# Optimization experiments

Measured on AMD Instinct MI355X. Metric: run time of the kernel, lower is better.

The kernel has to match this reference:

```python
import jax, jax.numpy as jnp
import numpy as np

D_MODEL = 1024
N_HEADS = 16
HEAD_DIM = D_MODEL // N_HEADS


def setup_inputs() -> dict:
    key = jax.random.key(0)
    ks = jax.random.split(key, 5)
    scale = 1.0 / np.sqrt(D_MODEL)
    x = jax.random.normal(ks[0], (2, 2048, D_MODEL), dtype=jnp.float32)
    Wq = jax.random.normal(ks[1], (D_MODEL, D_MODEL), dtype=jnp.float32) * scale
    Wk = jax.random.normal(ks[2], (D_MODEL, D_MODEL), dtype=jnp.float32) * scale
    Wv = jax.random.normal(ks[3], (D_MODEL, D_MODEL), dtype=jnp.float32) * scale
    Wo = jax.random.normal(ks[4], (D_MODEL, D_MODEL), dtype=jnp.float32) * scale
    return {"x": x, "Wq": Wq, "Wk": Wk, "Wv": Wv, "Wo": Wo}


def reference(x, Wq, Wk, Wv, Wo):
    # x: [B, S, D]; weights stored as [out, in] like nn.Linear -> y = x @ W.T
    B, S, D = x.shape
    H, Hd = N_HEADS, HEAD_DIM
    attn_scale = 1.0 / np.sqrt(Hd)

    def split_heads(t):  # [B,S,D] -> [B,H,S,Hd]
        return t.reshape(B, S, H, Hd).transpose(0, 2, 1, 3)

    q = split_heads(x @ Wq.T)
    k = split_heads(x @ Wk.T)
    v = split_heads(x @ Wv.T)

    scores = jnp.einsum('bhqd,bhkd->bhqk', q, k) * attn_scale  # [B,H,S,S]
    causal = jnp.tril(jnp.ones((S, S), dtype=bool))
    scores = jnp.where(causal, scores, jnp.finfo(scores.dtype).min)
    attn = jax.nn.softmax(scores, axis=-1)
    out = jnp.einsum('bhqk,bhkd->bhqd', attn, v)  # [B,H,S,Hd]
    out = out.transpose(0, 2, 1, 3).reshape(B, S, D)
    return out @ Wo.T
```

## Files before the change

kernel.cpp:

```cpp
#include <hip/hip_runtime.h>
#include <hip/hip_bf16.h>

typedef __attribute__((ext_vector_type(8))) __bf16 bf16x8;
typedef __attribute__((ext_vector_type(4))) __bf16 bf16x4;
typedef __attribute__((ext_vector_type(4))) float f32x4;

#define D_MODEL 1024
#define S_LEN   2048
#define BATCH   2
#define NH      16
#define HD      64
#define MROWS   (BATCH * S_LEN)

#define EXP2F(x) __builtin_amdgcn_exp2f(x)

__global__ __launch_bounds__(256) void cvt_bf16(const float* __restrict__ in,
                                                __bf16* __restrict__ out, int n4) {
    int i = blockIdx.x * 256 + threadIdx.x;
    if (i < n4) {
        float4 v = ((const float4*)in)[i];
        bf16x4 o = {(__bf16)v.x, (__bf16)v.y, (__bf16)v.z, (__bf16)v.w};
        ((bf16x4*)out)[i] = o;
    }
}

__global__ __launch_bounds__(256) void cvt_w3(const float* __restrict__ Wq,
                                              const float* __restrict__ Wk,
                                              const float* __restrict__ Wv,
                                              __bf16* __restrict__ out) {
    const int per = (D_MODEL * D_MODEL) / 4;
    int i = blockIdx.x * 256 + threadIdx.x;
    int sel = i / per;
    int off = i - sel * per;
    const float* src = (sel == 0) ? Wq : (sel == 1) ? Wk : Wv;
    float4 v = ((const float4*)src)[off];
    bf16x4 o = {(__bf16)v.x, (__bf16)v.y, (__bf16)v.z, (__bf16)v.w};
    ((bf16x4*)out)[i] = o;
}

__device__ __forceinline__ void g2l16(const void* g, __bf16* l) {
    __builtin_amdgcn_global_load_lds((const __attribute__((address_space(1))) void*)g,
                                     (__attribute__((address_space(3))) void*)l, 16, 0, 0);
}

__global__ __launch_bounds__(256) void gemm_qkv(const __bf16* __restrict__ A,
                                                const __bf16* __restrict__ W,
                                                __bf16* __restrict__ Qb,
                                                __bf16* __restrict__ Kq,
                                                __bf16* __restrict__ VTb,
                                                float qs) {
    __shared__ __bf16 sa[128 * 64];
    __shared__ __bf16 sb[128 * 64];

    const int t    = threadIdx.x;
    const int lane = t & 63;
    const int wid  = t >> 6;
    const int lr   = lane & 15;
    const int lg   = lane >> 4;
    const int wr   = wid >> 1;
    const int wc   = wid & 1;
    const int K    = D_MODEL;
    const int m0   = blockIdx.y * 128;
    const int n0   = blockIdx.x * 128;

    const __bf16* Ab = A + (size_t)m0 * K;
    const __bf16* Wb = W + (size_t)n0 * K;

    f32x4 acc[4][4];
#pragma unroll
    for (int m = 0; m < 4; m++)
#pragma unroll
        for (int n = 0; n < 4; n++) acc[m][n] = (f32x4){0.f, 0.f, 0.f, 0.f};

    for (int k0 = 0; k0 < K; k0 += 64) {
#pragma unroll
        for (int i = 0; i < 4; i++) {
            int ca = i * 256 + t;
            int row = ca >> 3;
            int sc  = ((ca & 7) ^ (row & 7)) * 8;
            g2l16(&Ab[(size_t)row * K + k0 + sc], &sa[ca * 8]);
            g2l16(&Wb[(size_t)row * K + k0 + sc], &sb[ca * 8]);
        }
        __syncthreads();

        bf16x8 af[4][2], bfr[4][2];
#pragma unroll
        for (int m = 0; m < 4; m++) {
            const int row = wr * 64 + m * 16 + lr;
#pragma unroll
            for (int kc = 0; kc < 2; kc++)
                af[m][kc] = *(const bf16x8*)&sa[row * 64 + (((kc * 4 + lg) ^ (lr & 7)) * 8)];
        }
#pragma unroll
        for (int n = 0; n < 4; n++) {
            const int row = wc * 64 + n * 16 + lr;
#pragma unroll
            for (int kc = 0; kc < 2; kc++)
                bfr[n][kc] = *(const bf16x8*)&sb[row * 64 + (((kc * 4 + lg) ^ (lr & 7)) * 8)];
        }
#pragma unroll
        for (int m = 0; m < 4; m++)
#pragma unroll
            for (int n = 0; n < 4; n++)
#pragma unroll
                for (int kc = 0; kc < 2; kc++)
                    acc[m][n] = __builtin_amdgcn_mfma_f32_16x16x32_bf16(af[m][kc], bfr[n][kc], acc[m][n], 0, 0, 0);
        __syncthreads();
    }

#pragma unroll
    for (int m = 0; m < 4; m++) {
#pragma unroll
        for (int n = 0; n < 4; n++) {
#pragma unroll
            for (int j = 0; j < 4; j++) {
                int row = m0 + wr * 64 + m * 16 + lg * 4 + j;
                int col = n0 + wc * 64 + n * 16 + lr;
                float v = acc[m][n][j];
                if (col < 1024) {
                    Qb[(size_t)row * D_MODEL + col] = (__bf16)(v * qs);
                } else if (col < 2048) {
                    Kq[(size_t)row * D_MODEL + col - 1024] = (__bf16)v;
                } else {
                    int c2 = col - 2048;
                    int b = row >> 11, s = row & 2047;
                    int h = c2 >> 6, d = c2 & 63;
                    VTb[(((size_t)(b * NH + h) * HD + d) << 11) + s] = (__bf16)v;
                }
            }
        }
    }
}

__global__ __launch_bounds__(256) void gemm_out(const __bf16* __restrict__ A,
                                                const __bf16* __restrict__ W,
                                                float* __restrict__ C,
                                                int M, int N, int K) {
    __shared__ __bf16 sa[128 * 64];
    __shared__ __bf16 sb[64 * 64];

    const int t    = threadIdx.x;
    const int lane = t & 63;
    const int wid  = t >> 6;
    const int lr   = lane & 15;
    const int lg   = lane >> 4;
    const int wr   = wid >> 1;
    const int wc   = wid & 1;
    const int m0   = blockIdx.y * 128;
    const int n0   = blockIdx.x * 64;

    const __bf16* Ab = A + (size_t)m0 * K;
    const __bf16* Wb = W + (size_t)n0 * K;

    f32x4 acc[4][2];
#pragma unroll
    for (int m = 0; m < 4; m++)
#pragma unroll
        for (int n = 0; n < 2; n++) acc[m][n] = (f32x4){0.f, 0.f, 0.f, 0.f};

    for (int k0 = 0; k0 < K; k0 += 64) {
#pragma unroll
        for (int i = 0; i < 4; i++) {
            int ca = i * 256 + t;
            int row = ca >> 3;
            int sc  = ((ca & 7) ^ (row & 7)) * 8;
            g2l16(&Ab[(size_t)row * K + k0 + sc], &sa[ca * 8]);
        }
#pragma unroll
        for (int i = 0; i < 2; i++) {
            int ca = i * 256 + t;
            int row = ca >> 3;
            int sc  = ((ca & 7) ^ (row & 7)) * 8;
            g2l16(&Wb[(size_t)row * K + k0 + sc], &sb[ca * 8]);
        }
        __syncthreads();

        bf16x8 af[4][2], bfr[2][2];
#pragma unroll
        for (int m = 0; m < 4; m++) {
            const int row = wr * 64 + m * 16 + lr;
#pragma unroll
            for (int kc = 0; kc < 2; kc++)
                af[m][kc] = *(const bf16x8*)&sa[row * 64 + (((kc * 4 + lg) ^ (lr & 7)) * 8)];
        }
#pragma unroll
        for (int n = 0; n < 2; n++) {
            const int row = wc * 32 + n * 16 + lr;
#pragma unroll
            for (int kc = 0; kc < 2; kc++)
                bfr[n][kc] = *(const bf16x8*)&sb[row * 64 + (((kc * 4 + lg) ^ (lr & 7)) * 8)];
        }
#pragma unroll
        for (int m = 0; m < 4; m++)
#pragma unroll
            for (int n = 0; n < 2; n++)
#pragma unroll
                for (int kc = 0; kc < 2; kc++)
                    acc[m][n] = __builtin_amdgcn_mfma_f32_16x16x32_bf16(af[m][kc], bfr[n][kc], acc[m][n], 0, 0, 0);
        __syncthreads();
    }

#pragma unroll
    for (int m = 0; m < 4; m++)
#pragma unroll
        for (int n = 0; n < 2; n++)
#pragma unroll
            for (int j = 0; j < 4; j++) {
                int row = m0 + wr * 64 + m * 16 + lg * 4 + j;
                int col = n0 + wc * 32 + n * 16 + lr;
                C[(size_t)row * N + col] = acc[m][n][j];
            }
}

__global__ __launch_bounds__(256) void attn_fwd(const __bf16* __restrict__ Q,
                                                const __bf16* __restrict__ Kb,
                                                const __bf16* __restrict__ VT,
                                                __bf16* __restrict__ O) {
    __shared__ __bf16 kt[2][64 * 64];
    __shared__ __bf16 vt[2][64 * 64];
    __shared__ __bf16 pt[4][16][72];

    const int t    = threadIdx.x;
    const int lane = t & 63;
    const int wid  = t >> 6;
    const int lr   = lane & 15;
    const int lg   = lane >> 4;
    const int bid  = blockIdx.x;
    const int qb   = 31 - (bid >> 5);
    const int bh   = bid & 31;
    const int b    = bh >> 4;
    const int h    = bh & 15;
    const int col  = h * HD;

    const size_t qrow = (size_t)b * S_LEN + qb * 64 + wid * 16;
    const int q_lo = qb * 64 + wid * 16 + lg * 4;
    const __bf16* Kbase = Kb + (size_t)b * S_LEN * D_MODEL + col;
    const __bf16* Vbase = VT + (size_t)bh * HD * S_LEN;

    const int ca0 = t, ca1 = t + 256;
    const int r0 = ca0 >> 3, s0 = ((ca0 & 7) ^ (r0 & 7)) * 8;
    const int r1 = ca1 >> 3, s1 = ((ca1 & 7) ^ (r1 & 7)) * 8;

    bf16x8 qf[2];
#pragma unroll
    for (int c = 0; c < 2; c++)
        qf[c] = *(const bf16x8*)&Q[(qrow + lr) * D_MODEL + col + c * 32 + lg * 8];

    f32x4 o[4];
#pragma unroll
    for (int n = 0; n < 4; n++) o[n] = (f32x4){0.f, 0.f, 0.f, 0.f};
    float psum[4] = {0.f, 0.f, 0.f, 0.f};

    g2l16(&Kbase[(size_t)r0 * D_MODEL + s0], &kt[0][ca0 * 8]);
    g2l16(&Kbase[(size_t)r1 * D_MODEL + s1], &kt[0][ca1 * 8]);
    g2l16(&Vbase[(size_t)r0 * S_LEN + s0],   &vt[0][ca0 * 8]);
    g2l16(&Vbase[(size_t)r1 * S_LEN + s1],   &vt[0][ca1 * 8]);
    __syncthreads();

    for (int kvt = 0; kvt <= qb; kvt++) {
        const int kv0 = kvt * 64;
        const int cur = kvt & 1;
        const bool diag = (kvt == qb);

        if (kvt < qb) {
            const int nb = cur ^ 1;
            const int kv1 = kv0 + 64;
            g2l16(&Kbase[(size_t)(kv1 + r0) * D_MODEL + s0], &kt[nb][ca0 * 8]);
            g2l16(&Kbase[(size_t)(kv1 + r1) * D_MODEL + s1], &kt[nb][ca1 * 8]);
            g2l16(&Vbase[(size_t)r0 * S_LEN + kv1 + s0],     &vt[nb][ca0 * 8]);
            g2l16(&Vbase[(size_t)r1 * S_LEN + kv1 + s1],     &vt[nb][ca1 * 8]);
        }

        f32x4 s[4];
        __builtin_amdgcn_s_setprio(1);
#pragma unroll
        for (int tt = 0; tt < 4; tt++) {
            s[tt] = (f32x4){0.f, 0.f, 0.f, 0.f};
#pragma unroll
            for (int c = 0; c < 2; c++) {
                const int row = tt * 16 + lr;
                bf16x8 kf = *(const bf16x8*)&kt[cur][row * 64 + (((c * 4 + lg) ^ (lr & 7)) * 8)];
                s[tt] = __builtin_amdgcn_mfma_f32_16x16x32_bf16(qf[c], kf, s[tt], 0, 0, 0);
            }
        }
        __builtin_amdgcn_s_setprio(0);

        if (diag) {
#pragma unroll
            for (int tt = 0; tt < 4; tt++) {
                int kg = kv0 + tt * 16 + lr;
#pragma unroll
                for (int j = 0; j < 4; j++)
                    if (kg > q_lo + j) s[tt][j] = -1e30f;
            }
        }

#pragma unroll
        for (int tt = 0; tt < 4; tt++) {
#pragma unroll
            for (int j = 0; j < 4; j++) {
                float p = EXP2F(s[tt][j]);
                psum[j] += p;
                pt[wid][lg * 4 + j][tt * 16 + lr] = (__bf16)p;
            }
        }

        asm volatile("s_waitcnt lgkmcnt(0)" ::: "memory");
        __builtin_amdgcn_sched_barrier(0);

        __builtin_amdgcn_s_setprio(1);
#pragma unroll
        for (int c = 0; c < 2; c++) {
            bf16x8 pa = *(const bf16x8*)&pt[wid][lr][c * 32 + lg * 8];
#pragma unroll
            for (int n = 0; n < 4; n++) {
                const int d = n * 16 + lr;
                bf16x8 vf = *(const bf16x8*)&vt[cur][d * 64 + (((c * 4 + lg) ^ (lr & 7)) * 8)];
                o[n] = __builtin_amdgcn_mfma_f32_16x16x32_bf16(pa, vf, o[n], 0, 0, 0);
            }
        }
        __builtin_amdgcn_s_setprio(0);

        __syncthreads();
    }

#pragma unroll
    for (int j = 0; j < 4; j++) {
#pragma unroll
        for (int off = 1; off < 16; off <<= 1)
            psum[j] += __shfl_xor(psum[j], off, 64);
        psum[j] = 1.0f / psum[j];
    }

#pragma unroll
    for (int n = 0; n < 4; n++) {
#pragma unroll
        for (int j = 0; j < 4; j++) {
            float val = o[n][j] * psum[j];
            O[(qrow + lg * 4 + j) * D_MODEL + col + n * 16 + lr] = (__bf16)val;
        }
    }
}

extern "C" void kernel_launch(void* const* d_in, const int* in_sizes, int n_in,
                              void* d_out, int out_size, void* d_ws, size_t ws_size,
                              hipStream_t stream) {
    const float* x  = (const float*)d_in[0];
    const float* Wq = (const float*)d_in[1];
    const float* Wk = (const float*)d_in[2];
    const float* Wv = (const float*)d_in[3];
    const float* Wo = (const float*)d_in[4];
    float* out = (float*)d_out;

    const size_t XE = (size_t)MROWS * D_MODEL;
    const size_t WE = (size_t)D_MODEL * D_MODEL;
    __bf16* xb  = (__bf16*)d_ws;
    __bf16* Qb  = xb + XE;
    __bf16* Kq  = Qb + XE;
    __bf16* VTb = Kq + XE;
    __bf16* AO  = xb;

    __bf16* wqkv = (__bf16*)d_out;
    __bf16* wob  = Qb;

    cvt_bf16<<<(int)(XE / 4 / 256), 256, 0, stream>>>(x, xb, (int)(XE / 4));
    cvt_w3<<<(int)(3 * WE / 4 / 256), 256, 0, stream>>>(Wq, Wk, Wv, wqkv);

    const float qs = 0.125f * 1.44269504088896340736f;
    gemm_qkv<<<dim3(3 * D_MODEL / 128, MROWS / 128), 256, 0, stream>>>(xb, wqkv, Qb, Kq, VTb, qs);

    attn_fwd<<<1024, 256, 0, stream>>>(Qb, Kq, VTb, AO);

    cvt_bf16<<<(int)(WE / 4 / 256), 256, 0, stream>>>(Wo, wob, (int)(WE / 4));
    gemm_out<<<dim3(D_MODEL / 64, MROWS / 128), 256, 0, stream>>>(AO, wob, out, MROWS, D_MODEL, D_MODEL);
}
```

Measured before the change: 118.3 us.

## Process 128 query rows per attention block and fuse input conversions

Each attention wave now handles two 16-row query chunks, so one block covers 128 query rows. Every K/V tile loaded into LDS is therefore reused across twice as many queries, and the grid shrinks from 1024 to 512 blocks. The x and Wq/Wk/Wv fp32-to-bf16 conversions are merged into a single launch to save one kernel launch. The trade-offs are higher register pressure, fewer blocks to balance the uneven causal work, and some waves spending MFMA work on fully masked diagonal tiles.

```diff
diff --git a/kernel.cpp b/kernel.cpp
--- a/kernel.cpp
+++ b/kernel.cpp
@@ -24,18 +24,30 @@
     }
 }
 
-__global__ __launch_bounds__(256) void cvt_w3(const float* __restrict__ Wq,
-                                              const float* __restrict__ Wk,
-                                              const float* __restrict__ Wv,
-                                              __bf16* __restrict__ out) {
-    const int per = (D_MODEL * D_MODEL) / 4;
+__global__ __launch_bounds__(256) void cvt_all(const float* __restrict__ x,
+                                               const float* __restrict__ Wq,
+                                               const float* __restrict__ Wk,
+                                               const float* __restrict__ Wv,
+                                               __bf16* __restrict__ xb,
+                                               __bf16* __restrict__ wqkv) {
+    const int nx = (MROWS * D_MODEL) / 4;
+    const int nw = (D_MODEL * D_MODEL) / 4;
     int i = blockIdx.x * 256 + threadIdx.x;
-    int sel = i / per;
-    int off = i - sel * per;
-    const float* src = (sel == 0) ? Wq : (sel == 1) ? Wk : Wv;
-    float4 v = ((const float4*)src)[off];
+    const float* src;
+    __bf16* dst;
+    int si, di;
+    if (i < nx) {
+        src = x; si = i; dst = xb; di = i;
+    } else {
+        int k = i - nx;
+        int sel = k / nw;
+        si = k - sel * nw;
+        src = (sel == 0) ? Wq : (sel == 1) ? Wk : Wv;
+        dst = wqkv; di = k;
+    }
+    float4 v = ((const float4*)src)[si];
     bf16x4 o = {(__bf16)v.x, (__bf16)v.y, (__bf16)v.z, (__bf16)v.w};
-    ((bf16x4*)out)[i] = o;
+    ((bf16x4*)dst)[di] = o;
 }
 
 __device__ __forceinline__ void g2l16(const void* g, __bf16* l) {
@@ -226,14 +238,13 @@
     const int lr   = lane & 15;
     const int lg   = lane >> 4;
     const int bid  = blockIdx.x;
-    const int qb   = 31 - (bid >> 5);
+    const int qb   = 15 - (bid >> 5);
     const int bh   = bid & 31;
     const int b    = bh >> 4;
     const int h    = bh & 15;
     const int col  = h * HD;
 
-    const size_t qrow = (size_t)b * S_LEN + qb * 64 + wid * 16;
-    const int q_lo = qb * 64 + wid * 16 + lg * 4;
+    const size_t qrowb = (size_t)b * S_LEN + qb * 128 + wid * 32;
     const __bf16* Kbase = Kb + (size_t)b * S_LEN * D_MODEL + col;
     const __bf16* Vbase = VT + (size_t)bh * HD * S_LEN;
 
@@ -241,15 +252,19 @@
     const int r0 = ca0 >> 3, s0 = ((ca0 & 7) ^ (r0 & 7)) * 8;
     const int r1 = ca1 >> 3, s1 = ((ca1 & 7) ^ (r1 & 7)) * 8;
 
-    bf16x8 qf[2];
-#pragma unroll
-    for (int c = 0; c < 2; c++)
-        qf[c] = *(const bf16x8*)&Q[(qrow + lr) * D_MODEL + col + c * 32 + lg * 8];
-
-    f32x4 o[4];
-#pragma unroll
-    for (int n = 0; n < 4; n++) o[n] = (f32x4){0.f, 0.f, 0.f, 0.f};
-    float psum[4] = {0.f, 0.f, 0.f, 0.f};
+    bf16x8 qf[2][2];
+#pragma unroll
+    for (int hc = 0; hc < 2; hc++)
+#pragma unroll
+        for (int c = 0; c < 2; c++)
+            qf[hc][c] = *(const bf16x8*)&Q[(qrowb + hc * 16 + lr) * D_MODEL + col + c * 32 + lg * 8];
+
+    f32x4 o[2][4];
+#pragma unroll
+    for (int hc = 0; hc < 2; hc++)
+#pragma unroll
+        for (int n = 0; n < 4; n++) o[hc][n] = (f32x4){0.f, 0.f, 0.f, 0.f};
+    float psum[2][4] = {{0.f, 0.f, 0.f, 0.f}, {0.f, 0.f, 0.f, 0.f}};
 
     g2l16(&Kbase[(size_t)r0 * D_MODEL + s0], &kt[0][ca0 * 8]);
     g2l16(&Kbase[(size_t)r1 * D_MODEL + s1], &kt[0][ca1 * 8]);
@@ -257,12 +272,12 @@
     g2l16(&Vbase[(size_t)r1 * S_LEN + s1],   &vt[0][ca1 * 8]);
     __syncthreads();
 
-    for (int kvt = 0; kvt <= qb; kvt++) {
+    const int nkv = 2 * qb + 2;
+    for (int kvt = 0; kvt < nkv; kvt++) {
         const int kv0 = kvt * 64;
         const int cur = kvt & 1;
-        const bool diag = (kvt == qb);
-
-        if (kvt < qb) {
+
+        if (kvt < nkv - 1) {
             const int nb = cur ^ 1;
             const int kv1 = kv0 + 64;
             g2l16(&Kbase[(size_t)(kv1 + r0) * D_MODEL + s0], &kt[nb][ca0 * 8]);
@@ -271,75 +286,90 @@
             g2l16(&Vbase[(size_t)r1 * S_LEN + kv1 + s1],     &vt[nb][ca1 * 8]);
         }
 
-        f32x4 s[4];
+        f32x4 s[2][4];
         __builtin_amdgcn_s_setprio(1);
 #pragma unroll
         for (int tt = 0; tt < 4; tt++) {
-            s[tt] = (f32x4){0.f, 0.f, 0.f, 0.f};
+            s[0][tt] = (f32x4){0.f, 0.f, 0.f, 0.f};
+            s[1][tt] = (f32x4){0.f, 0.f, 0.f, 0.f};
 #pragma unroll
             for (int c = 0; c < 2; c++) {
                 const int row = tt * 16 + lr;
                 bf16x8 kf = *(const bf16x8*)&kt[cur][row * 64 + (((c * 4 + lg) ^ (lr & 7)) * 8)];
-                s[tt] = __builtin_amdgcn_mfma_f32_16x16x32_bf16(qf[c], kf, s[tt], 0, 0, 0);
+                s[0][tt] = __builtin_amdgcn_mfma_f32_16x16x32_bf16(qf[0][c], kf, s[0][tt], 0, 0, 0);
+                s[1][tt] = __builtin_amdgcn_mfma_f32_16x16x32_bf16(qf[1][c], kf, s[1][tt], 0, 0, 0);
             }
         }
         __builtin_amdgcn_s_setprio(0);
 
-        if (diag) {
-#pragma unroll
-            for (int tt = 0; tt < 4; tt++) {
-                int kg = kv0 + tt * 16 + lr;
-#pragma unroll
-                for (int j = 0; j < 4; j++)
-                    if (kg > q_lo + j) s[tt][j] = -1e30f;
-            }
-        }
-
-#pragma unroll
-        for (int tt = 0; tt < 4; tt++) {
-#pragma unroll
-            for (int j = 0; j < 4; j++) {
-                float p = EXP2F(s[tt][j]);
-                psum[j] += p;
-                pt[wid][lg * 4 + j][tt * 16 + lr] = (__bf16)p;
-            }
-        }
-
-        asm volatile("s_waitcnt lgkmcnt(0)" ::: "memory");
-        __builtin_amdgcn_sched_barrier(0);
-
-        __builtin_amdgcn_s_setprio(1);
-#pragma unroll
-        for (int c = 0; c < 2; c++) {
-            bf16x8 pa = *(const bf16x8*)&pt[wid][lr][c * 32 + lg * 8];
+        bf16x8 vf[2][4];
+#pragma unroll
+        for (int c = 0; c < 2; c++)
 #pragma unroll
             for (int n = 0; n < 4; n++) {
                 const int d = n * 16 + lr;
-                bf16x8 vf = *(const bf16x8*)&vt[cur][d * 64 + (((c * 4 + lg) ^ (lr & 7)) * 8)];
-                o[n] = __builtin_amdgcn_mfma_f32_16x16x32_bf16(pa, vf, o[n], 0, 0, 0);
-            }
-        }
-        __builtin_amdgcn_s_setprio(0);
+                vf[c][n] = *(const bf16x8*)&vt[cur][d * 64 + (((c * 4 + lg) ^ (lr & 7)) * 8)];
+            }
+
+#pragma unroll
+        for (int hc = 0; hc < 2; hc++) {
+            const int cb = qb * 128 + wid * 32 + hc * 16;
+            if (kv0 + 63 > cb) {
+#pragma unroll
+                for (int tt = 0; tt < 4; tt++) {
+                    int kg = kv0 + tt * 16 + lr;
+#pragma unroll
+                    for (int j = 0; j < 4; j++)
+                        if (kg > cb + lg * 4 + j) s[hc][tt][j] = -1e30f;
+                }
+            }
+
+#pragma unroll
+            for (int tt = 0; tt < 4; tt++) {
+#pragma unroll
+                for (int j = 0; j < 4; j++) {
+                    float p = EXP2F(s[hc][tt][j]);
+                    psum[hc][j] += p;
+                    pt[wid][lg * 4 + j][tt * 16 + lr] = (__bf16)p;
+                }
+            }
+
+            asm volatile("s_waitcnt lgkmcnt(0)" ::: "memory");
+            __builtin_amdgcn_sched_barrier(0);
+
+            __builtin_amdgcn_s_setprio(1);
+#pragma unroll
+            for (int c = 0; c < 2; c++) {
+                bf16x8 pa = *(const bf16x8*)&pt[wid][lr][c * 32 + lg * 8];
+#pragma unroll
+                for (int n = 0; n < 4; n++)
+                    o[hc][n] = __builtin_amdgcn_mfma_f32_16x16x32_bf16(pa, vf[c][n], o[hc][n], 0, 0, 0);
+            }
+            __builtin_amdgcn_s_setprio(0);
+        }
 
         __syncthreads();
     }
 
 #pragma unroll
-    for (int j = 0; j < 4; j++) {
-#pragma unroll
-        for (int off = 1; off < 16; off <<= 1)
-            psum[j] += __shfl_xor(psum[j], off, 64);
-        psum[j] = 1.0f / psum[j];
-    }
-
-#pragma unroll
-    for (int n = 0; n < 4; n++) {
+    for (int hc = 0; hc < 2; hc++)
 #pragma unroll
         for (int j = 0; j < 4; j++) {
-            float val = o[n][j] * psum[j];
-            O[(qrow + lg * 4 + j) * D_MODEL + col + n * 16 + lr] = (__bf16)val;
-        }
-    }
+#pragma unroll
+            for (int off = 1; off < 16; off <<= 1)
+                psum[hc][j] += __shfl_xor(psum[hc][j], off, 64);
+            psum[hc][j] = 1.0f / psum[hc][j];
+        }
+
+#pragma unroll
+    for (int hc = 0; hc < 2; hc++)
+#pragma unroll
+        for (int n = 0; n < 4; n++)
+#pragma unroll
+            for (int j = 0; j < 4; j++) {
+                float val = o[hc][n][j] * psum[hc][j];
+                O[(qrowb + hc * 16 + lg * 4 + j) * D_MODEL + col + n * 16 + lr] = (__bf16)val;
+            }
 }
 
 extern "C" void kernel_launch(void* const* d_in, const int* in_sizes, int n_in,
@@ -363,13 +393,13 @@
     __bf16* wqkv = (__bf16*)d_out;
     __bf16* wob  = Qb;
 
-    cvt_bf16<<<(int)(XE / 4 / 256), 256, 0, stream>>>(x, xb, (int)(XE / 4));
-    cvt_w3<<<(int)(3 * WE / 4 / 256), 256, 0, stream>>>(Wq, Wk, Wv, wqkv);
+    const int ncv = (int)(XE / 4 + 3 * WE / 4);
+    cvt_all<<<(ncv + 255) / 256, 256, 0, stream>>>(x, Wq, Wk, Wv, xb, wqkv);
 
     const float qs = 0.125f * 1.44269504088896340736f;
     gemm_qkv<<<dim3(3 * D_MODEL / 128, MROWS / 128), 256, 0, stream>>>(xb, wqkv, Qb, Kq, VTb, qs);
 
-    attn_fwd<<<1024, 256, 0, stream>>>(Qb, Kq, VTb, AO);
+    attn_fwd<<<512, 256, 0, stream>>>(Qb, Kq, VTb, AO);
 
     cvt_bf16<<<(int)(WE / 4 / 256), 256, 0, stream>>>(Wo, wob, (int)(WE / 4));
     gemm_out<<<dim3(D_MODEL / 64, MROWS / 128), 256, 0, stream>>>(AO, wob, out, MROWS, D_MODEL, D_MODEL);
```

Measured after the change: 131.9 us. 1.12x slower.

## Transpose S tile in attention for vectorized P stores; merge conversion kernels

Applied to the files above, without the earlier changes.

Swaps the MFMA operand order in the QK^T product so each lane holds four consecutive key scores for one query row. P can then be written to LDS as a single 4-element vector per tile into an XOR-swizzled unpadded buffer, instead of scalar stores. The row sum becomes one scalar per lane, reduced across lane groups and redistributed with shuffles at the end. The x and Wq/Wk/Wv fp32-to-bf16 conversions are merged into one launch to save a kernel launch. The risk is correctness in the swizzled P layout and the transposed causal mask.

```diff
diff --git a/kernel.cpp b/kernel.cpp
--- a/kernel.cpp
+++ b/kernel.cpp
@@ -24,18 +24,30 @@
     }
 }
 
-__global__ __launch_bounds__(256) void cvt_w3(const float* __restrict__ Wq,
-                                              const float* __restrict__ Wk,
-                                              const float* __restrict__ Wv,
-                                              __bf16* __restrict__ out) {
-    const int per = (D_MODEL * D_MODEL) / 4;
+__global__ __launch_bounds__(256) void cvt_all(const float* __restrict__ x,
+                                               const float* __restrict__ Wq,
+                                               const float* __restrict__ Wk,
+                                               const float* __restrict__ Wv,
+                                               __bf16* __restrict__ xb,
+                                               __bf16* __restrict__ wqkv) {
+    const int nx = (MROWS * D_MODEL) / 4;
+    const int nw = (D_MODEL * D_MODEL) / 4;
     int i = blockIdx.x * 256 + threadIdx.x;
-    int sel = i / per;
-    int off = i - sel * per;
-    const float* src = (sel == 0) ? Wq : (sel == 1) ? Wk : Wv;
-    float4 v = ((const float4*)src)[off];
+    const float* src;
+    __bf16* dst;
+    int si, di;
+    if (i < nx) {
+        src = x; si = i; dst = xb; di = i;
+    } else {
+        int k = i - nx;
+        int sel = k / nw;
+        si = k - sel * nw;
+        src = (sel == 0) ? Wq : (sel == 1) ? Wk : Wv;
+        dst = wqkv; di = k;
+    }
+    float4 v = ((const float4*)src)[si];
     bf16x4 o = {(__bf16)v.x, (__bf16)v.y, (__bf16)v.z, (__bf16)v.w};
-    ((bf16x4*)out)[i] = o;
+    ((bf16x4*)dst)[di] = o;
 }
 
 __device__ __forceinline__ void g2l16(const void* g, __bf16* l) {
@@ -218,7 +230,7 @@
                                                 __bf16* __restrict__ O) {
     __shared__ __bf16 kt[2][64 * 64];
     __shared__ __bf16 vt[2][64 * 64];
-    __shared__ __bf16 pt[4][16][72];
+    __shared__ __bf16 pt[4][16][64];
 
     const int t    = threadIdx.x;
     const int lane = t & 63;
@@ -233,9 +245,10 @@
     const int col  = h * HD;
 
     const size_t qrow = (size_t)b * S_LEN + qb * 64 + wid * 16;
-    const int q_lo = qb * 64 + wid * 16 + lg * 4;
+    const int qg = qb * 64 + wid * 16 + lr;
     const __bf16* Kbase = Kb + (size_t)b * S_LEN * D_MODEL + col;
     const __bf16* Vbase = VT + (size_t)bh * HD * S_LEN;
+    const int pswz = (lr & 7) * 8;
 
     const int ca0 = t, ca1 = t + 256;
     const int r0 = ca0 >> 3, s0 = ((ca0 & 7) ^ (r0 & 7)) * 8;
@@ -249,7 +262,7 @@
     f32x4 o[4];
 #pragma unroll
     for (int n = 0; n < 4; n++) o[n] = (f32x4){0.f, 0.f, 0.f, 0.f};
-    float psum[4] = {0.f, 0.f, 0.f, 0.f};
+    float psum = 0.f;
 
     g2l16(&Kbase[(size_t)r0 * D_MODEL + s0], &kt[0][ca0 * 8]);
     g2l16(&Kbase[(size_t)r1 * D_MODEL + s1], &kt[0][ca1 * 8]);
@@ -280,7 +293,7 @@
             for (int c = 0; c < 2; c++) {
                 const int row = tt * 16 + lr;
                 bf16x8 kf = *(const bf16x8*)&kt[cur][row * 64 + (((c * 4 + lg) ^ (lr & 7)) * 8)];
-                s[tt] = __builtin_amdgcn_mfma_f32_16x16x32_bf16(qf[c], kf, s[tt], 0, 0, 0);
+                s[tt] = __builtin_amdgcn_mfma_f32_16x16x32_bf16(kf, qf[c], s[tt], 0, 0, 0);
             }
         }
         __builtin_amdgcn_s_setprio(0);
@@ -288,21 +301,20 @@
         if (diag) {
 #pragma unroll
             for (int tt = 0; tt < 4; tt++) {
-                int kg = kv0 + tt * 16 + lr;
+                int kg = kv0 + tt * 16 + lg * 4;
 #pragma unroll
                 for (int j = 0; j < 4; j++)
-                    if (kg > q_lo + j) s[tt][j] = -1e30f;
+                    if (kg + j > qg) s[tt][j] = -1e30f;
             }
         }
 
 #pragma unroll
         for (int tt = 0; tt < 4; tt++) {
-#pragma unroll
-            for (int j = 0; j < 4; j++) {
-                float p = EXP2F(s[tt][j]);
-                psum[j] += p;
-                pt[wid][lg * 4 + j][tt * 16 + lr] = (__bf16)p;
-            }
+            float p0 = EXP2F(s[tt][0]), p1 = EXP2F(s[tt][1]);
+            float p2 = EXP2F(s[tt][2]), p3 = EXP2F(s[tt][3]);
+            psum += (p0 + p1) + (p2 + p3);
+            bf16x4 pw = {(__bf16)p0, (__bf16)p1, (__bf16)p2, (__bf16)p3};
+            *(bf16x4*)&pt[wid][lr][(tt * 16 + lg * 4) ^ pswz] = pw;
         }
 
         asm volatile("s_waitcnt lgkmcnt(0)" ::: "memory");
@@ -311,7 +323,7 @@
         __builtin_amdgcn_s_setprio(1);
 #pragma unroll
         for (int c = 0; c < 2; c++) {
-            bf16x8 pa = *(const bf16x8*)&pt[wid][lr][c * 32 + lg * 8];
+            bf16x8 pa = *(const bf16x8*)&pt[wid][lr][(c * 32 + lg * 8) ^ pswz];
 #pragma unroll
             for (int n = 0; n < 4; n++) {
                 const int d = n * 16 + lr;
@@ -324,19 +336,18 @@
         __syncthreads();
     }
 
-#pragma unroll
-    for (int j = 0; j < 4; j++) {
-#pragma unroll
-        for (int off = 1; off < 16; off <<= 1)
-            psum[j] += __shfl_xor(psum[j], off, 64);
-        psum[j] = 1.0f / psum[j];
-    }
+    psum += __shfl_xor(psum, 16, 64);
+    psum += __shfl_xor(psum, 32, 64);
+    float inv = 1.0f / psum;
+    float invj[4];
+#pragma unroll
+    for (int j = 0; j < 4; j++) invj[j] = __shfl(inv, lg * 4 + j, 64);
 
 #pragma unroll
     for (int n = 0; n < 4; n++) {
 #pragma unroll
         for (int j = 0; j < 4; j++) {
-            float val = o[n][j] * psum[j];
+            float val = o[n][j] * invj[j];
             O[(qrow + lg * 4 + j) * D_MODEL + col + n * 16 + lr] = (__bf16)val;
         }
     }
@@ -363,8 +374,8 @@
     __bf16* wqkv = (__bf16*)d_out;
     __bf16* wob  = Qb;
 
-    cvt_bf16<<<(int)(XE / 4 / 256), 256, 0, stream>>>(x, xb, (int)(XE / 4));
-    cvt_w3<<<(int)(3 * WE / 4 / 256), 256, 0, stream>>>(Wq, Wk, Wv, wqkv);
+    const int ncv = (int)(XE / 4 + 3 * WE / 4);
+    cvt_all<<<(ncv + 255) / 256, 256, 0, stream>>>(x, Wq, Wk, Wv, xb, wqkv);
 
     const float qs = 0.125f * 1.44269504088896340736f;
     gemm_qkv<<<dim3(3 * D_MODEL / 128, MROWS / 128), 256, 0, stream>>>(xb, wqkv, Qb, Kq, VTb, qs);
```

After: 113.9 us. -3.7%, faster.
